# Kernel tuning notes

Hardware: AMD Instinct MI355X
Metric: run time of the kernel (lower is better)

Reference implementation:

```python
import jax, jax.numpy as jnp
import numpy as np

N, T, V, F, K, FO = 8, 64, 200, 64, 3, 64


def setup_inputs() -> dict:
    key = jax.random.key(0)
    k1, k2, k3, k4 = jax.random.split(key, 4)
    x = jax.random.normal(k1, (N, T, V, F), dtype=jnp.float32)
    Att = jax.random.uniform(k2, (N, V, V), dtype=jnp.float32)
    S = jax.random.uniform(k3, (N, T, V, V), dtype=jnp.float32)
    Theta = jax.random.normal(k4, (K, F, FO), dtype=jnp.float32) * 0.1
    return {"x": x, "Att": Att, "S": S, "Theta": Theta}


def reference(x, Att, S, Theta):
    # x: (N,T,V,F); Att: (N,V,V); S: (N,T,V,V); Theta: (K,F,FO)
    n, t, v, f = x.shape
    k_order = Theta.shape[0]
    # symmetrize S by elementwise min with its transpose (last two dims)
    S = jnp.minimum(S, jnp.swapaxes(S, -1, -2))
    eye = jnp.eye(v, dtype=x.dtype)
    # D = diag_embed(sum(A, dim=1)) per timestep -> column sums over axis 2
    d = jnp.sum(S, axis=2)                      # (N,T,V)
    L = d[..., :, None] * eye - S               # (N,T,V,V), D - A
    L_t = L - eye                               # tilde-L
    # Chebyshev recursion (elementwise, matching original code exactly)
    polys = [jnp.broadcast_to(eye, (1, 1, v, v)), L_t][:k_order]
    for _ in range(2, k_order):
        polys.append(2.0 * L_t * polys[-1] - polys[-2])
    Att_b = Att[:, None]                        # (N,1,V,V), broadcast over T
    out = jnp.zeros((n, t, v, Theta.shape[-1]), dtype=x.dtype)
    for kk in range(k_order):
        T_k_att = polys[kk] * Att_b             # (N,T,V,V) (broadcast for k=0)
        # rhs = T_k_att^T @ x : sum over vertex u
        rhs = jnp.einsum('...uv,...uf->...vf', T_k_att, x)  # (N,T,V,F)
        out = out + rhs @ Theta[kk]             # (N,T,V,FO)
    return jax.nn.relu(out)
```

## Files before the change

kernel.cpp:

```cpp
#include <hip/hip_runtime.h>

namespace {

typedef __attribute__((ext_vector_type(8)))  short          short8;
typedef __attribute__((ext_vector_type(8)))  unsigned short u16x8;
typedef __attribute__((ext_vector_type(4)))  unsigned short u16x4;
typedef __attribute__((ext_vector_type(4)))  float          f32x4;
typedef __attribute__((ext_vector_type(8)))  _Float16       half8;
typedef __attribute__((ext_vector_type(4)))  _Float16       half4;

constexpr int V  = 200;
constexpr int F  = 64;
constexpr int NT = 512;
constexpr int VP = 208;

constexpr size_t WS_MC   = 0;
constexpr size_t WS_XTF  = 47710208;
constexpr size_t WS_ATTF = 62390272;
constexpr size_t WS_THT  = 63135744;
constexpr size_t WS_D    = 63160320;
constexpr size_t WS_ADG  = 63586304;

__device__ __forceinline__ unsigned short f2bf(float x) {
    union { float f; unsigned u; } c; c.f = x;
    unsigned r = c.u + 0x7FFF + ((c.u >> 16) & 1);
    return (unsigned short)(r >> 16);
}

__global__ __launch_bounds__(256)
void prep_all(const float* __restrict__ S,
              const float* __restrict__ Att,
              const float* __restrict__ x,
              const float* __restrict__ Theta,
              _Float16* __restrict__ Mc,
              _Float16* __restrict__ attF,
              _Float16* __restrict__ xTf,
              unsigned short* __restrict__ thT,
              float* __restrict__ d_ws,
              float* __restrict__ adiag)
{
    __shared__ __align__(16) char smem[30464];
    const int b = blockIdx.x, n = b >> 6, tid = threadIdx.x;

    if (blockIdx.y == 28) {
        _Float16* xs = (_Float16*)smem;
        const float* __restrict__ xp = x + (size_t)b * (V * F);
        for (int idx = tid; idx < 224 * 16; idx += 256) {
            const int u = idx >> 4, fg = idx & 15;
            half4 w = (half4)(_Float16)0.f;
            if (u < V) {
                const float4 v4 = *(const float4*)&xp[u * F + 4 * fg];
                w[0] = (_Float16)v4.x; w[1] = (_Float16)v4.y;
                w[2] = (_Float16)v4.z; w[3] = (_Float16)v4.w;
            }
            *(half4*)&xs[u * 68 + 4 * fg] = w;
        }
        __syncthreads();
        _Float16* xo = xTf + (size_t)b * 14336;
        for (int it = 0; it < 7; ++it) {
            const int wid = tid + 256 * it;
            const int frag = wid >> 6, lane = wid & 63;
            const int kt = frag >> 2, ft = frag & 3;
            const int q = lane >> 4, ln = lane & 15;
            half8 w;
            #pragma unroll
            for (int j = 0; j < 8; ++j)
                w[j] = xs[(32 * kt + 8 * q + j) * 68 + 16 * ft + ln];
            *(half8*)&xo[frag * 512 + lane * 8] = w;
        }
        if (b < 3) {
            const int k = b;
            __syncthreads();
            float* T = (float*)smem;
            for (int idx = tid; idx < 4096; idx += 256)
                T[(idx >> 6) * 65 + (idx & 63)] = Theta[k * 4096 + idx];
            __syncthreads();
            for (int idx = tid; idx < 4096; idx += 256) {
                const int fo = idx >> 6, f = idx & 63;
                thT[k * 4096 + fo * 64 + f] = f2bf(T[f * 65 + fo]);
            }
        }
        return;
    }

    float (*As)[33] = (float(*)[33])smem;
    float (*Bs)[33] = (float(*)[33])(smem + 4224);
    float (*Ts)[33] = (float(*)[33])(smem + 8448);
    float (*Us)[33] = (float(*)[33])(smem + 12672);
    float (*Ms)[33] = (float(*)[33])(smem + 16896);

    int rem = blockIdx.y, ti = 0;
    while (rem >= 7 - ti) { rem -= 7 - ti; ++ti; }
    const int tj = ti + rem;
    const bool diag = (ti == tj);

    const float* __restrict__ Sp = S   + (size_t)b * (V * V);
    const float* __restrict__ Ap = Att + (size_t)n * (V * V);

    const int r = tid >> 3, cg = tid & 7, c0 = 4 * cg;

    {
        const int gr = 32 * ti + r, gc = 32 * tj + c0;
        float4 a = make_float4(0.f, 0.f, 0.f, 0.f);
        float4 t = make_float4(0.f, 0.f, 0.f, 0.f);
        if (gr < V && gc < V) {
            a = *(const float4*)&Sp[gr * V + gc];
            t = *(const float4*)&Ap[gr * V + gc];
        }
        As[r][c0+0] = a.x; As[r][c0+1] = a.y; As[r][c0+2] = a.z; As[r][c0+3] = a.w;
        Ts[r][c0+0] = t.x; Ts[r][c0+1] = t.y; Ts[r][c0+2] = t.z; Ts[r][c0+3] = t.w;
        if (!diag) {
            const int hr = 32 * tj + r, hc = 32 * ti + c0;
            float4 bb = make_float4(0.f, 0.f, 0.f, 0.f);
            float4 uu = make_float4(0.f, 0.f, 0.f, 0.f);
            if (hr < V && hc < V) {
                bb = *(const float4*)&Sp[hr * V + hc];
                uu = *(const float4*)&Ap[hr * V + hc];
            }
            Bs[r][c0+0] = bb.x; Bs[r][c0+1] = bb.y; Bs[r][c0+2] = bb.z; Bs[r][c0+3] = bb.w;
            Us[r][c0+0] = uu.x; Us[r][c0+1] = uu.y; Us[r][c0+2] = uu.z; Us[r][c0+3] = uu.w;
        }
    }
    __syncthreads();

    {
        float rs = 0.f;
        #pragma unroll
        for (int e = 0; e < 4; ++e) {
            const int c = c0 + e;
            const float tw = diag ? As[c][r] : Bs[c][r];
            const float m = fminf(As[r][c], tw);
            Ms[r][c] = m;
            rs += m;
        }
        rs += __shfl_xor(rs, 1); rs += __shfl_xor(rs, 2); rs += __shfl_xor(rs, 4);
        const int vg = 32 * ti + r;
        if (cg == 0 && vg < V) {
            const float extra = diag ? (-1.0f - As[r][r]) : 0.0f;
            atomicAdd(&d_ws[b * VP + vg], rs + extra);
            if (diag) adiag[n * VP + vg] = Ts[r][r];
        }
    }
    __syncthreads();

    if (!diag) {
        float ts = 0.f;
        #pragma unroll
        for (int e = 0; e < 4; ++e) ts += Ms[c0 + e][r];
        ts += __shfl_xor(ts, 1); ts += __shfl_xor(ts, 2); ts += __shfl_xor(ts, 4);
        if (cg == 0 && 32 * tj + r < V)
            atomicAdd(&d_ws[b * VP + 32 * tj + r], ts);
    }

    const int jh = tid & 1, lane = (tid >> 1) & 63, sub = tid >> 7;
    const int rr = lane & 15, qq = lane >> 4;
    const int vl = sub * 16 + rr;
    const int ub = 8 * qq + 4 * jh;
    const bool wAtt = ((b & 63) == 0);

    if (2 * ti + sub < 13) {
        half4 wm, wa;
        #pragma unroll
        for (int e = 0; e < 4; ++e) {
            const int ul = ub + e;
            wm[e] = (_Float16)Ms[vl][ul];
            const float att = diag ? Ts[ul][vl] : Us[ul][vl];
            wa[e] = (diag && ul == vl) ? (_Float16)0.f : (_Float16)att;
        }
        const size_t base = ((size_t)(b * 13 + 2 * ti + sub) * 7 + tj) * 512 + lane * 8 + jh * 4;
        *(half4*)&Mc[base] = wm;
        if (wAtt) {
            const size_t ab = ((size_t)(n * 13 + 2 * ti + sub) * 7 + tj) * 512 + lane * 8 + jh * 4;
            *(half4*)&attF[ab] = wa;
        }
    }
    if (!diag && 2 * tj + sub < 13) {
        half4 wm, wa;
        #pragma unroll
        for (int e = 0; e < 4; ++e) {
            const int ul = ub + e;
            wm[e] = (_Float16)Ms[ul][vl];
            wa[e] = (_Float16)Ts[ul][vl];
        }
        const size_t base = ((size_t)(b * 13 + 2 * tj + sub) * 7 + ti) * 512 + lane * 8 + jh * 4;
        *(half4*)&Mc[base] = wm;
        if (wAtt) {
            const size_t ab = ((size_t)(n * 13 + 2 * tj + sub) * 7 + ti) * 512 + lane * 8 + jh * 4;
            *(half4*)&attF[ab] = wa;
        }
    }
}

__global__ __launch_bounds__(256, 4)
void cheb_stream(const float* __restrict__ x,
                 const _Float16* __restrict__ Mc,
                 const _Float16* __restrict__ attF,
                 const float* __restrict__ d_ws,
                 const float* __restrict__ adiag,
                 const unsigned short* __restrict__ thT,
                 const _Float16* __restrict__ xTf,
                 float* __restrict__ out)
{
    __shared__ __align__(16) char smem[29696];
    _Float16*       xTs = (_Float16*)smem;
    unsigned short* ys  = (unsigned short*)smem;
    unsigned short* ThS = (unsigned short*)(smem + 16128);
    float* dbuf = (float*)(smem + 28672);
    float* adb  = (float*)(smem + 29120);

    const int tid = threadIdx.x;
    const int ub_ = blockIdx.x;
    const int h   = (ub_ >> 3) & 1;
    const int b   = (ub_ & 7) | ((ub_ >> 4) << 3);
    const int n   = b >> 6;
    const int v0  = h * 112;

    const _Float16* __restrict__ xfp = xTf + (size_t)b * 14336;
    #pragma unroll
    for (int it = 0; it < 7; ++it) {
        const int o = it * 2048 + tid * 8;
        *(half8*)&xTs[o] = *(const half8*)&xfp[o];
    }
    if (tid < 112) {
        const int gv = v0 + tid;
        dbuf[tid] = (gv < VP) ? d_ws[b * VP + gv] : 0.f;
        adb[tid]  = (gv < VP) ? adiag[n * VP + gv] : 0.f;
    }

    const int wave = tid >> 6, lane = tid & 63, q = lane >> 4, ln = lane & 15;
    int myBase, myCnt;
    if (h == 0) { myCnt = (wave < 3) ? 2 : 1; myBase = 2 * wave; }
    else        { myCnt = (wave < 2) ? 2 : 1; myBase = (wave < 2) ? 2 * wave : 2 + wave; }

    const float* __restrict__ xp = x + (size_t)b * (V * F);
    float* __restrict__ op = out + (size_t)b * (V * F);

    f32x4 acc1[2][4], acc2[2][4];
    #pragma unroll
    for (int i = 0; i < 2; ++i)
        #pragma unroll
        for (int j = 0; j < 4; ++j) { acc1[i][j] = (f32x4)0.f; acc2[i][j] = (f32x4)0.f; }

    const size_t fb0 = ((size_t)(b * 13 + 7 * h + myBase) * 7) * 512 + lane * 8;
    const size_t fb1 = fb0 + 7 * 512;
    const size_t af0 = ((size_t)(n * 13 + 7 * h + myBase) * 7) * 512 + lane * 8;
    const size_t af1 = af0 + 7 * 512;

    half8 mc[2] = {}, ac[2] = {}, mn[2] = {}, an[2] = {};
    mc[0] = *(const half8*)&Mc[fb0];
    ac[0] = *(const half8*)&attF[af0];
    if (myCnt > 1) {
        mc[1] = *(const half8*)&Mc[fb1];
        ac[1] = *(const half8*)&attF[af1];
    }
    __syncthreads();

    #pragma unroll 1
    for (int kt = 0; kt < 7; ++kt) {
        if (kt < 6) {
            const size_t o = (size_t)(kt + 1) * 512;
            mn[0] = *(const half8*)&Mc[fb0 + o];
            an[0] = *(const half8*)&attF[af0 + o];
            if (myCnt > 1) {
                mn[1] = *(const half8*)&Mc[fb1 + o];
                an[1] = *(const half8*)&attF[af1 + o];
            }
        }
        half8 bfr[4];
        #pragma unroll
        for (int ft = 0; ft < 4; ++ft)
            bfr[ft] = *(const half8*)&xTs[(kt * 4 + ft) * 512 + lane * 8];
        #pragma unroll
        for (int vi = 0; vi < 2; ++vi) {
            if (vi < myCnt) {
                const half8 t  = mc[vi] * ac[vi];
                const half8 a1 = -t;
                const half8 a2 = (mc[vi] + mc[vi]) * t;
                #pragma unroll
                for (int ft = 0; ft < 4; ++ft) {
                    acc1[vi][ft] = __builtin_amdgcn_mfma_f32_16x16x32_f16(a1, bfr[ft], acc1[vi][ft], 0, 0, 0);
                    acc2[vi][ft] = __builtin_amdgcn_mfma_f32_16x16x32_f16(a2, bfr[ft], acc2[vi][ft], 0, 0, 0);
                }
            }
        }
        #pragma unroll
        for (int vi = 0; vi < 2; ++vi) { mc[vi] = mn[vi]; ac[vi] = an[vi]; }
    }

    f32x4 ot[2][4];
    #pragma unroll
    for (int i = 0; i < 2; ++i)
        #pragma unroll
        for (int j = 0; j < 4; ++j) ot[i][j] = (f32x4)0.f;

    #pragma unroll
    for (int pass = 0; pass < 3; ++pass) {
        const int k = (pass == 0) ? 1 : (pass == 1) ? 2 : 0;
        __syncthreads();

        if (k == 0) {
            for (int idx = tid; idx < 112 * 16; idx += 256) {
                const int vl = idx >> 4, fg = idx & 15;
                const int v = v0 + vl;
                u16x4 w; w[0] = 0; w[1] = 0; w[2] = 0; w[3] = 0;
                if (v < V) {
                    const float av = adb[vl];
                    const float4 xv = *(const float4*)&xp[v * F + 4 * fg];
                    w[0] = f2bf(av * xv.x); w[1] = f2bf(av * xv.y);
                    w[2] = f2bf(av * xv.z); w[3] = f2bf(av * xv.w);
                }
                *(u16x4*)&ys[vl * 72 + 4 * fg] = w;
            }
        } else {
            #pragma unroll
            for (int vi = 0; vi < 2; ++vi) {
                if (vi < myCnt) {
                    const int lt = myBase + vi;
                    #pragma unroll
                    for (int ft = 0; ft < 4; ++ft) {
                        const f32x4 a = (k == 1) ? acc1[vi][ft] : acc2[vi][ft];
                        #pragma unroll
                        for (int reg = 0; reg < 4; ++reg) {
                            const int vl = lt * 16 + 4 * q + reg;
                            const int v = v0 + vl;
                            float val = 0.f;
                            if (v < V) {
                                const float cc = dbuf[vl];
                                const float dc = ((k == 1) ? cc : (2.0f * cc * cc - 1.0f)) * adb[vl];
                                val = a[reg] + dc * xp[v * F + 16 * ft + ln];
                            }
                            ys[vl * 72 + 16 * ft + ln] = f2bf(val);
                        }
                    }
                }
            }
        }
        for (int idx = tid; idx < 512; idx += 256) {
            const int fo = idx >> 3, ch = idx & 7;
            *(u16x8*)&ThS[fo * 72 + 8 * ch] =
                *(const u16x8*)&thT[k * 4096 + fo * 64 + 8 * ch];
        }
        __syncthreads();
        #pragma unroll
        for (int vi = 0; vi < 2; ++vi) {
            if (vi < myCnt) {
                const int vrow = (myBase + vi) * 16 + ln;
                #pragma unroll
                for (int ks = 0; ks < 2; ++ks) {
                    const short8 af = *(const short8*)&ys[vrow * 72 + 32 * ks + 8 * q];
                    #pragma unroll
                    for (int fot = 0; fot < 4; ++fot) {
                        const short8 bf = *(const short8*)&ThS[(16 * fot + ln) * 72 + 32 * ks + 8 * q];
                        ot[vi][fot] = __builtin_amdgcn_mfma_f32_16x16x32_bf16(af, bf, ot[vi][fot], 0, 0, 0);
                    }
                }
            }
        }
    }

    #pragma unroll
    for (int vi = 0; vi < 2; ++vi) {
        if (vi < myCnt) {
            const int lt = myBase + vi;
            #pragma unroll
            for (int fot = 0; fot < 4; ++fot) {
                #pragma unroll
                for (int reg = 0; reg < 4; ++reg) {
                    const int v = v0 + lt * 16 + 4 * q + reg;
                    if (v < V)
                        op[v * F + 16 * fot + ln] = fmaxf(ot[vi][fot][reg], 0.f);
                }
            }
        }
    }
}

}

extern "C" void kernel_launch(void* const* d_in, const int* in_sizes, int n_in,
                              void* d_out, int out_size, void* d_ws, size_t ws_size,
                              hipStream_t stream) {
    const float* x     = (const float*)d_in[0];
    const float* Att   = (const float*)d_in[1];
    const float* S     = (const float*)d_in[2];
    const float* Theta = (const float*)d_in[3];
    float* out         = (float*)d_out;

    char* ws = (char*)d_ws;
    _Float16* Mc        = (_Float16*)(ws + WS_MC);
    _Float16* xTf       = (_Float16*)(ws + WS_XTF);
    _Float16* attF      = (_Float16*)(ws + WS_ATTF);
    unsigned short* thT = (unsigned short*)(ws + WS_THT);
    float* d_sum        = (float*)(ws + WS_D);
    float* adiag        = (float*)(ws + WS_ADG);

    hipMemsetAsync(d_sum, 0, (size_t)NT * VP * sizeof(float), stream);

    hipLaunchKernelGGL(prep_all, dim3(NT, 29), dim3(256), 0, stream,
                       S, Att, x, Theta, Mc, attF, xTf, thT, d_sum, adiag);
    hipLaunchKernelGGL(cheb_stream, dim3(2 * NT), dim3(256), 0, stream,
                       x, Mc, attF, d_sum, adiag, thT, xTf, out);
}
```

Baseline: 212.4 us.

## Batch prep over eight timesteps and compute degree sums in the main kernel

The prep kernel now loops over eight timesteps per block, so the grid shrinks to 64x29. Each block loads Att once and prefetches the next S tile into registers while the current one is processed. The atomic degree accumulation and the memset are removed; the consumer kernel instead rebuilds the degree from the fp16 Mc fragments it already loads, and prep stores only the S diagonal. This drops the atomics and a launch, at the cost of fewer, longer prep blocks and fp16 rounding in the degree sum.

```diff
diff --git a/kernel.cpp b/kernel.cpp
--- a/kernel.cpp
+++ b/kernel.cpp
@@ -8,6 +8,7 @@
 typedef __attribute__((ext_vector_type(4)))  float          f32x4;
 typedef __attribute__((ext_vector_type(8)))  _Float16       half8;
 typedef __attribute__((ext_vector_type(4)))  _Float16       half4;
+typedef __attribute__((ext_vector_type(2)))  _Float16       half2_t;
 
 constexpr int V  = 200;
 constexpr int F  = 64;
@@ -18,7 +19,7 @@
 constexpr size_t WS_XTF  = 47710208;
 constexpr size_t WS_ATTF = 62390272;
 constexpr size_t WS_THT  = 63135744;
-constexpr size_t WS_D    = 63160320;
+constexpr size_t WS_SD   = 63160320;
 constexpr size_t WS_ADG  = 63586304;
 
 __device__ __forceinline__ unsigned short f2bf(float x) {
@@ -36,48 +37,53 @@
               _Float16* __restrict__ attF,
               _Float16* __restrict__ xTf,
               unsigned short* __restrict__ thT,
-              float* __restrict__ d_ws,
+              float* __restrict__ sdiag,
               float* __restrict__ adiag)
 {
     __shared__ __align__(16) char smem[30464];
-    const int b = blockIdx.x, n = b >> 6, tid = threadIdx.x;
+    const int bx = blockIdx.x, tid = threadIdx.x;
 
     if (blockIdx.y == 28) {
         _Float16* xs = (_Float16*)smem;
-        const float* __restrict__ xp = x + (size_t)b * (V * F);
-        for (int idx = tid; idx < 224 * 16; idx += 256) {
-            const int u = idx >> 4, fg = idx & 15;
-            half4 w = (half4)(_Float16)0.f;
-            if (u < V) {
-                const float4 v4 = *(const float4*)&xp[u * F + 4 * fg];
-                w[0] = (_Float16)v4.x; w[1] = (_Float16)v4.y;
-                w[2] = (_Float16)v4.z; w[3] = (_Float16)v4.w;
-            }
-            *(half4*)&xs[u * 68 + 4 * fg] = w;
-        }
-        __syncthreads();
-        _Float16* xo = xTf + (size_t)b * 14336;
-        for (int it = 0; it < 7; ++it) {
-            const int wid = tid + 256 * it;
-            const int frag = wid >> 6, lane = wid & 63;
-            const int kt = frag >> 2, ft = frag & 3;
-            const int q = lane >> 4, ln = lane & 15;
-            half8 w;
-            #pragma unroll
-            for (int j = 0; j < 8; ++j)
-                w[j] = xs[(32 * kt + 8 * q + j) * 68 + 16 * ft + ln];
-            *(half8*)&xo[frag * 512 + lane * 8] = w;
-        }
-        if (b < 3) {
-            const int k = b;
+        for (int i = 0; i < 8; ++i) {
+            const int b = 8 * bx + i;
+            const float* __restrict__ xp = x + (size_t)b * (V * F);
             __syncthreads();
+            for (int idx = tid; idx < 224 * 16; idx += 256) {
+                const int u = idx >> 4, fg = idx & 15;
+                half4 w = (half4)(_Float16)0.f;
+                if (u < V) {
+                    const float4 v4 = *(const float4*)&xp[u * F + 4 * fg];
+                    w[0] = (_Float16)v4.x; w[1] = (_Float16)v4.y;
+                    w[2] = (_Float16)v4.z; w[3] = (_Float16)v4.w;
+                }
+                *(half4*)&xs[u * 68 + 4 * fg] = w;
+            }
+            __syncthreads();
+            _Float16* xo = xTf + (size_t)b * 14336;
+            for (int it = 0; it < 7; ++it) {
+                const int wid = tid + 256 * it;
+                const int frag = wid >> 6, lane = wid & 63;
+                const int kt = frag >> 2, ft = frag & 3;
+                const int q = lane >> 4, ln = lane & 15;
+                half8 w;
+                #pragma unroll
+                for (int j = 0; j < 8; ++j)
+                    w[j] = xs[(32 * kt + 8 * q + j) * 68 + 16 * ft + ln];
+                *(half8*)&xo[frag * 512 + lane * 8] = w;
+            }
+        }
+        if (bx == 0) {
             float* T = (float*)smem;
-            for (int idx = tid; idx < 4096; idx += 256)
-                T[(idx >> 6) * 65 + (idx & 63)] = Theta[k * 4096 + idx];
-            __syncthreads();
-            for (int idx = tid; idx < 4096; idx += 256) {
-                const int fo = idx >> 6, f = idx & 63;
-                thT[k * 4096 + fo * 64 + f] = f2bf(T[f * 65 + fo]);
+            for (int k = 0; k < 3; ++k) {
+                __syncthreads();
+                for (int idx = tid; idx < 4096; idx += 256)
+                    T[(idx >> 6) * 65 + (idx & 63)] = Theta[k * 4096 + idx];
+                __syncthreads();
+                for (int idx = tid; idx < 4096; idx += 256) {
+                    const int fo = idx >> 6, f = idx & 63;
+                    thT[k * 4096 + fo * 64 + f] = f2bf(T[f * 65 + fo]);
+                }
             }
         }
         return;
@@ -87,107 +93,100 @@
     float (*Bs)[33] = (float(*)[33])(smem + 4224);
     float (*Ts)[33] = (float(*)[33])(smem + 8448);
     float (*Us)[33] = (float(*)[33])(smem + 12672);
-    float (*Ms)[33] = (float(*)[33])(smem + 16896);
 
     int rem = blockIdx.y, ti = 0;
     while (rem >= 7 - ti) { rem -= 7 - ti; ++ti; }
     const int tj = ti + rem;
     const bool diag = (ti == tj);
 
-    const float* __restrict__ Sp = S   + (size_t)b * (V * V);
+    const int n = bx >> 3;
     const float* __restrict__ Ap = Att + (size_t)n * (V * V);
-
     const int r = tid >> 3, cg = tid & 7, c0 = 4 * cg;
 
     {
         const int gr = 32 * ti + r, gc = 32 * tj + c0;
-        float4 a = make_float4(0.f, 0.f, 0.f, 0.f);
         float4 t = make_float4(0.f, 0.f, 0.f, 0.f);
-        if (gr < V && gc < V) {
-            a = *(const float4*)&Sp[gr * V + gc];
-            t = *(const float4*)&Ap[gr * V + gc];
-        }
-        As[r][c0+0] = a.x; As[r][c0+1] = a.y; As[r][c0+2] = a.z; As[r][c0+3] = a.w;
+        if (gr < V && gc < V) t = *(const float4*)&Ap[gr * V + gc];
         Ts[r][c0+0] = t.x; Ts[r][c0+1] = t.y; Ts[r][c0+2] = t.z; Ts[r][c0+3] = t.w;
         if (!diag) {
             const int hr = 32 * tj + r, hc = 32 * ti + c0;
-            float4 bb = make_float4(0.f, 0.f, 0.f, 0.f);
             float4 uu = make_float4(0.f, 0.f, 0.f, 0.f);
-            if (hr < V && hc < V) {
-                bb = *(const float4*)&Sp[hr * V + hc];
-                uu = *(const float4*)&Ap[hr * V + hc];
-            }
-            Bs[r][c0+0] = bb.x; Bs[r][c0+1] = bb.y; Bs[r][c0+2] = bb.z; Bs[r][c0+3] = bb.w;
+            if (hr < V && hc < V) uu = *(const float4*)&Ap[hr * V + hc];
             Us[r][c0+0] = uu.x; Us[r][c0+1] = uu.y; Us[r][c0+2] = uu.z; Us[r][c0+3] = uu.w;
         }
     }
-    __syncthreads();
-
-    {
-        float rs = 0.f;
-        #pragma unroll
-        for (int e = 0; e < 4; ++e) {
-            const int c = c0 + e;
-            const float tw = diag ? As[c][r] : Bs[c][r];
-            const float m = fminf(As[r][c], tw);
-            Ms[r][c] = m;
-            rs += m;
-        }
-        rs += __shfl_xor(rs, 1); rs += __shfl_xor(rs, 2); rs += __shfl_xor(rs, 4);
-        const int vg = 32 * ti + r;
-        if (cg == 0 && vg < V) {
-            const float extra = diag ? (-1.0f - As[r][r]) : 0.0f;
-            atomicAdd(&d_ws[b * VP + vg], rs + extra);
-            if (diag) adiag[n * VP + vg] = Ts[r][r];
-        }
-    }
-    __syncthreads();
-
-    if (!diag) {
-        float ts = 0.f;
-        #pragma unroll
-        for (int e = 0; e < 4; ++e) ts += Ms[c0 + e][r];
-        ts += __shfl_xor(ts, 1); ts += __shfl_xor(ts, 2); ts += __shfl_xor(ts, 4);
-        if (cg == 0 && 32 * tj + r < V)
-            atomicAdd(&d_ws[b * VP + 32 * tj + r], ts);
-    }
+
+    float4 pa, pb;
+    auto loadS = [&](int b) {
+        const float* __restrict__ Sp = S + (size_t)b * (V * V);
+        const int gr = 32 * ti + r, gc = 32 * tj + c0;
+        pa = make_float4(0.f, 0.f, 0.f, 0.f);
+        if (gr < V && gc < V) pa = *(const float4*)&Sp[gr * V + gc];
+        if (!diag) {
+            const int hr = 32 * tj + r, hc = 32 * ti + c0;
+            pb = make_float4(0.f, 0.f, 0.f, 0.f);
+            if (hr < V && hc < V) pb = *(const float4*)&Sp[hr * V + hc];
+        }
+    };
+    loadS(8 * bx);
 
     const int jh = tid & 1, lane = (tid >> 1) & 63, sub = tid >> 7;
     const int rr = lane & 15, qq = lane >> 4;
     const int vl = sub * 16 + rr;
-    const int ub = 8 * qq + 4 * jh;
-    const bool wAtt = ((b & 63) == 0);
-
-    if (2 * ti + sub < 13) {
-        half4 wm, wa;
-        #pragma unroll
-        for (int e = 0; e < 4; ++e) {
-            const int ul = ub + e;
-            wm[e] = (_Float16)Ms[vl][ul];
-            const float att = diag ? Ts[ul][vl] : Us[ul][vl];
-            wa[e] = (diag && ul == vl) ? (_Float16)0.f : (_Float16)att;
-        }
-        const size_t base = ((size_t)(b * 13 + 2 * ti + sub) * 7 + tj) * 512 + lane * 8 + jh * 4;
-        *(half4*)&Mc[base] = wm;
-        if (wAtt) {
-            const size_t ab = ((size_t)(n * 13 + 2 * ti + sub) * 7 + tj) * 512 + lane * 8 + jh * 4;
-            *(half4*)&attF[ab] = wa;
-        }
-    }
-    if (!diag && 2 * tj + sub < 13) {
-        half4 wm, wa;
-        #pragma unroll
-        for (int e = 0; e < 4; ++e) {
-            const int ul = ub + e;
-            wm[e] = (_Float16)Ms[ul][vl];
-            wa[e] = (_Float16)Ts[ul][vl];
-        }
-        const size_t base = ((size_t)(b * 13 + 2 * tj + sub) * 7 + ti) * 512 + lane * 8 + jh * 4;
-        *(half4*)&Mc[base] = wm;
-        if (wAtt) {
-            const size_t ab = ((size_t)(n * 13 + 2 * tj + sub) * 7 + ti) * 512 + lane * 8 + jh * 4;
-            *(half4*)&attF[ab] = wa;
-        }
+    const int ub2 = 8 * qq + 4 * jh;
+
+    #pragma unroll 1
+    for (int i = 0; i < 8; ++i) {
+        const int b = 8 * bx + i;
+        As[r][c0+0] = pa.x; As[r][c0+1] = pa.y; As[r][c0+2] = pa.z; As[r][c0+3] = pa.w;
+        if (!diag) {
+            Bs[r][c0+0] = pb.x; Bs[r][c0+1] = pb.y; Bs[r][c0+2] = pb.z; Bs[r][c0+3] = pb.w;
+        }
+        __syncthreads();
+        if (i < 7) loadS(b + 1);
+
+        if (diag && cg == 0) {
+            const int vg = 32 * ti + r;
+            if (vg < VP) {
+                sdiag[b * VP + vg] = As[r][r];
+                if ((b & 63) == 0) adiag[n * VP + vg] = Ts[r][r];
+            }
+        }
+
+        const bool wAtt = ((b & 63) == 0);
+        if (2 * ti + sub < 13) {
+            half4 wm, wa;
+            #pragma unroll
+            for (int e = 0; e < 4; ++e) {
+                const int ul = ub2 + e;
+                const float mB = diag ? As[ul][vl] : Bs[ul][vl];
+                wm[e] = (_Float16)fminf(As[vl][ul], mB);
+                const float att = diag ? Ts[ul][vl] : Us[ul][vl];
+                wa[e] = (diag && ul == vl) ? (_Float16)0.f : (_Float16)att;
+            }
+            const size_t base = ((size_t)(b * 13 + 2 * ti + sub) * 7 + tj) * 512 + lane * 8 + jh * 4;
+            *(half4*)&Mc[base] = wm;
+            if (wAtt) {
+                const size_t ab = ((size_t)(n * 13 + 2 * ti + sub) * 7 + tj) * 512 + lane * 8 + jh * 4;
+                *(half4*)&attF[ab] = wa;
+            }
+        }
+        if (!diag && 2 * tj + sub < 13) {
+            half4 wm, wa;
+            #pragma unroll
+            for (int e = 0; e < 4; ++e) {
+                const int ul = ub2 + e;
+                wm[e] = (_Float16)fminf(Bs[vl][ul], As[ul][vl]);
+                wa[e] = (_Float16)Ts[ul][vl];
+            }
+            const size_t base = ((size_t)(b * 13 + 2 * tj + sub) * 7 + ti) * 512 + lane * 8 + jh * 4;
+            *(half4*)&Mc[base] = wm;
+            if (wAtt) {
+                const size_t ab = ((size_t)(n * 13 + 2 * tj + sub) * 7 + ti) * 512 + lane * 8 + jh * 4;
+                *(half4*)&attF[ab] = wa;
+            }
+        }
+        __syncthreads();
     }
 }
 
@@ -195,18 +194,19 @@
 void cheb_stream(const float* __restrict__ x,
                  const _Float16* __restrict__ Mc,
                  const _Float16* __restrict__ attF,
-                 const float* __restrict__ d_ws,
+                 const float* __restrict__ sdiag,
                  const float* __restrict__ adiag,
                  const unsigned short* __restrict__ thT,
                  const _Float16* __restrict__ xTf,
                  float* __restrict__ out)
 {
-    __shared__ __align__(16) char smem[29696];
+    __shared__ __align__(16) char smem[30080];
     _Float16*       xTs = (_Float16*)smem;
     unsigned short* ys  = (unsigned short*)smem;
     unsigned short* ThS = (unsigned short*)(smem + 16128);
     float* dbuf = (float*)(smem + 28672);
     float* adb  = (float*)(smem + 29120);
+    float* sdb  = (float*)(smem + 29568);
 
     const int tid = threadIdx.x;
     const int ub_ = blockIdx.x;
@@ -223,8 +223,8 @@
     }
     if (tid < 112) {
         const int gv = v0 + tid;
-        dbuf[tid] = (gv < VP) ? d_ws[b * VP + gv] : 0.f;
-        adb[tid]  = (gv < VP) ? adiag[n * VP + gv] : 0.f;
+        adb[tid] = (gv < VP) ? adiag[n * VP + gv] : 0.f;
+        sdb[tid] = (gv < VP) ? sdiag[b * VP + gv] : 0.f;
     }
 
     const int wave = tid >> 6, lane = tid & 63, q = lane >> 4, ln = lane & 15;
@@ -254,6 +254,14 @@
         ac[1] = *(const half8*)&attF[af1];
     }
     __syncthreads();
+
+    float dsum0 = 0.f, dsum1 = 0.f;
+    auto hsum = [](half8 m) -> float {
+        const half2_t a = __builtin_shufflevector(m, m, 0, 1) + __builtin_shufflevector(m, m, 2, 3);
+        const half2_t c = __builtin_shufflevector(m, m, 4, 5) + __builtin_shufflevector(m, m, 6, 7);
+        const half2_t s = a + c;
+        return (float)s[0] + (float)s[1];
+    };
 
     #pragma unroll 1
     for (int kt = 0; kt < 7; ++kt) {
@@ -270,6 +278,10 @@
         #pragma unroll
         for (int ft = 0; ft < 4; ++ft)
             bfr[ft] = *(const half8*)&xTs[(kt * 4 + ft) * 512 + lane * 8];
+
+        dsum0 += hsum(mc[0]);
+        if (myCnt > 1) dsum1 += hsum(mc[1]);
+
         #pragma unroll
         for (int vi = 0; vi < 2; ++vi) {
             if (vi < myCnt) {
@@ -285,6 +297,17 @@
         }
         #pragma unroll
         for (int vi = 0; vi < 2; ++vi) { mc[vi] = mn[vi]; ac[vi] = an[vi]; }
+    }
+
+    dsum0 += __shfl_xor(dsum0, 16); dsum0 += __shfl_xor(dsum0, 32);
+    dsum1 += __shfl_xor(dsum1, 16); dsum1 += __shfl_xor(dsum1, 32);
+    if (lane < 16) {
+        const int vl0 = myBase * 16 + lane;
+        dbuf[vl0] = dsum0 - 1.0f - sdb[vl0];
+        if (myCnt > 1) {
+            const int vl1 = (myBase + 1) * 16 + lane;
+            dbuf[vl1] = dsum1 - 1.0f - sdb[vl1];
+        }
     }
 
     f32x4 ot[2][4];
@@ -391,13 +414,11 @@
     _Float16* xTf       = (_Float16*)(ws + WS_XTF);
     _Float16* attF      = (_Float16*)(ws + WS_ATTF);
     unsigned short* thT = (unsigned short*)(ws + WS_THT);
-    float* d_sum        = (float*)(ws + WS_D);
+    float* sdiag        = (float*)(ws + WS_SD);
     float* adiag        = (float*)(ws + WS_ADG);
 
-    hipMemsetAsync(d_sum, 0, (size_t)NT * VP * sizeof(float), stream);
-
-    hipLaunchKernelGGL(prep_all, dim3(NT, 29), dim3(256), 0, stream,
-                       S, Att, x, Theta, Mc, attF, xTf, thT, d_sum, adiag);
+    hipLaunchKernelGGL(prep_all, dim3(64, 29), dim3(256), 0, stream,
+                       S, Att, x, Theta, Mc, attF, xTf, thT, sdiag, adiag);
     hipLaunchKernelGGL(cheb_stream, dim3(2 * NT), dim3(256), 0, stream,
-                       x, Mc, attF, d_sum, adiag, thT, xTf, out);
+                       x, Mc, attF, sdiag, adiag, thT, xTf, out);
 }
```

Result: slower. 261.9 us (+23.3%).
